# Optimization experiments

Measured on AMD Instinct MI355X. Metric: run time of the kernel, lower is better.

The kernel has to match this reference:

```python
import jax, jax.numpy as jnp
import numpy as np
from jax import lax

CR = 16        # opt.cr (temporal dim)
HEADS = 4      # num_heads
DIM = 64       # dim == channel count c
B = 2          # true batch; input batch = B*CR
H = W = 128


def setup_inputs() -> dict:
    key = jax.random.key(0)
    k1, k2, k3, k4 = jax.random.split(key, 4)
    return {
        "x": jax.random.normal(k1, (B * CR, DIM, H, W), jnp.float32),
        "ln_weight": jnp.ones((DIM,), jnp.float32),
        "ln_bias": jnp.zeros((DIM,), jnp.float32),
        "qkv_w": jax.random.normal(k2, (3 * CR, CR), jnp.float32) * 0.05,   # 1x1 conv
        "dw_w": jax.random.normal(k3, (3 * CR, 1, 3, 3), jnp.float32) * 0.1,  # depthwise 3x3
        "proj_w": jax.random.normal(k4, (DIM, DIM), jnp.float32) * 0.05,   # 1x1 conv
        "temperature": jnp.ones((HEADS, 1, 1), jnp.float32),
    }


def reference(x, ln_weight, ln_bias, qkv_w, dw_w, proj_w, temperature):
    b, c, h, w = x.shape
    Bt = b // CR
    # WithBias LayerNorm over channel dim (per spatial location), eps=1e-5
    mu = jnp.mean(x, axis=1, keepdims=True)
    var = jnp.mean(jnp.square(x - mu), axis=1, keepdims=True)
    xn = (x - mu) / jnp.sqrt(var + 1e-5)
    xn = xn * ln_weight[None, :, None, None] + ln_bias[None, :, None, None]
    # (B*cr, c, h, w) -> (B, cr, c, h, w) -> (B*c, cr, h, w)
    x_in = xn.reshape(Bt, CR, c, h, w).transpose(0, 2, 1, 3, 4).reshape(Bt * c, CR, h, w)
    # 1x1 qkv conv (no bias)
    qkv = jnp.einsum('oc,bchw->bohw', qkv_w, x_in)
    # depthwise 3x3 conv, padding 1
    qkv = lax.conv_general_dilated(qkv, dw_w, (1, 1), 'SAME',
                                   feature_group_count=3 * CR,
                                   dimension_numbers=('NCHW', 'OIHW', 'NCHW'))
    q, k, v = jnp.split(qkv, 3, axis=1)
    ch = CR // HEADS  # per-head channel dim

    def heads(t):
        return t.reshape(Bt * c, HEADS, ch, h * w)

    def l2n(t):
        n = jnp.sqrt(jnp.sum(jnp.square(t), axis=-1, keepdims=True))
        return t / jnp.maximum(n, 1e-12)

    q, k, v = heads(q), heads(k), heads(v)
    q, k = l2n(q), l2n(k)
    # transposed (channel) attention: small ch x ch scores
    attn = jnp.einsum('bhcn,bhdn->bhcd', q, k) * temperature[None]
    attn = jax.nn.softmax(attn, axis=-1)
    out = jnp.einsum('bhcd,bhdn->bhcn', attn, v)  # (B*c, heads, ch, hw)
    # (B*c, cr, h, w) -> (B, c, cr, h, w) -> (B*cr, c, h, w)
    out = out.reshape(Bt * c, CR, h, w).reshape(Bt, c, CR, h, w)
    out = out.transpose(0, 2, 1, 3, 4).reshape(b, c, h, w)
    # 1x1 project_out
    return jnp.einsum('oc,bchw->bohw', proj_w, out)
```

## Files before the change

### kernel.cpp

```cpp
#include <hip/hip_runtime.h>
#include <hip/hip_fp16.h>

__device__ __forceinline__ float2 h2f2(unsigned int u) {
  return __half22float2(__builtin_bit_cast(__half2, u));
}
__device__ __forceinline__ unsigned int f2h2(float a, float b) {
  return __builtin_bit_cast(unsigned int, __floats2half2_rn(a, b));
}

#if __has_builtin(__builtin_amdgcn_fdot2)
typedef _Float16 h2v __attribute__((ext_vector_type(2)));
__device__ __forceinline__ float fdot2(unsigned int a, unsigned int b, float c) {
  return __builtin_amdgcn_fdot2(__builtin_bit_cast(h2v, a),
                                __builtin_bit_cast(h2v, b), c, false);
}
#else
__device__ __forceinline__ float fdot2(unsigned int a, unsigned int b, float c) {
  float2 fa = h2f2(a), fb = h2f2(b);
  return fmaf(fa.y, fb.y, fmaf(fa.x, fb.x, c));
}
#endif

__global__ __launch_bounds__(256) void k_stats(const float2* __restrict__ x2,
                                               float4* __restrict__ stats4) {
  int id = blockIdx.x * 256 + threadIdx.x;
  int bb = id >> 13;
  int jp = id & 8191;
  const float2* xp = x2 + ((size_t)bb << 19) + jp;
  float s0 = 0.f, q0 = 0.f, s1 = 0.f, q1 = 0.f;
#pragma unroll
  for (int ci = 0; ci < 64; ++ci) {
    float2 v = xp[(size_t)ci << 13];
    s0 += v.x; q0 = fmaf(v.x, v.x, q0);
    s1 += v.y; q1 = fmaf(v.y, v.y, q1);
  }
  float mu0 = s0 * (1.f / 64.f), mu1 = s1 * (1.f / 64.f);
  float4 r;
  r.x = mu0; r.y = rsqrtf(fmaf(-mu0, mu0, q0 * (1.f / 64.f)) + 1e-5f);
  r.z = mu1; r.w = rsqrtf(fmaf(-mu1, mu1, q1 * (1.f / 64.f)) + 1e-5f);
  stats4[id] = r;
}

__global__ __launch_bounds__(256) void k_wpack(
    const float* __restrict__ qkvw, const float* __restrict__ dww,
    const float* __restrict__ projw, unsigned int* __restrict__ qkvpk,
    unsigned int* __restrict__ dwpk, unsigned int* __restrict__ projpk) {
  int t = blockIdx.x * 256 + threadIdx.x;
  if (t < 2048) {
    int o = t >> 5, c2 = t & 31;
    projpk[t] = f2h2(projw[(o << 6) + 2 * c2], projw[(o << 6) + 2 * c2 + 1]);
  } else if (t < 2432) {
    int i = t - 2048;
    int ch = i >> 3, tp = i & 7;
    qkvpk[i] = f2h2(qkvw[(ch << 4) + 2 * tp], qkvw[(ch << 4) + 2 * tp + 1]);
  } else if (t < 2648) {
    int i = t - 2432;
    int pl = i / 9, k = i - pl * 9;
    dwpk[i] = f2h2(dww[18 * pl + k], dww[18 * pl + 9 + k]);
  }
}

__global__ __launch_bounds__(256, 6) void k_fused(
    const float* __restrict__ x, const float2* __restrict__ stats2,
    const float* __restrict__ lnw, const float* __restrict__ lnb,
    const unsigned int* __restrict__ qkvpk, const unsigned int* __restrict__ dwpk,
    unsigned int* __restrict__ vbuf, float* __restrict__ Sacc,
    float* __restrict__ Nacc) {
  __shared__ unsigned int pre[4896];
  int tid = threadIdx.x;
  int bc = blockIdx.y, bt = bc >> 6, ci = bc & 63;
  int tx0 = (blockIdx.x & 3) << 5, ty0 = (blockIdx.x >> 2) << 4;
  float lw = lnw[ci], lb = lnb[ci];

  unsigned int wc[3][8];
  int waddr[3];
  {
    size_t xci = ((size_t)(bt * 1024 + ci)) << 14;
    int sbase = bt << 18;
#pragma unroll
    for (int it = 0; it < 3; ++it) {
      int pos = tid + (it << 8);
      bool act = pos < 612;
      int hy = pos / 34, hx = pos - hy * 34;
      int gy = ty0 + hy - 1, gx = tx0 + hx - 1;
      bool ok = act && ((unsigned)gy < 128u) && ((unsigned)gx < 128u);
      waddr[it] = act ? (hy * 34 + hx) : -1;
      int gp = (gy << 7) + gx;
#pragma unroll
      for (int tp = 0; tp < 8; ++tp) {
        unsigned int w = 0;
        if (ok) {
          float x0 = x[xci + ((size_t)(2 * tp) << 20) + gp];
          float x1 = x[xci + ((size_t)(2 * tp + 1) << 20) + gp];
          float2 s0 = stats2[sbase + (2 * tp) * 16384 + gp];
          float2 s1 = stats2[sbase + (2 * tp + 1) * 16384 + gp];
          w = f2h2(fmaf((x0 - s0.x) * s0.y, lw, lb),
                   fmaf((x1 - s1.x) * s1.y, lw, lb));
        }
        wc[it][tp] = w;
      }
    }
  }

  int iy = tid >> 4, jx = tid & 15;
  int dwbase = iy * 34 + 2 * jx;

  for (int m = 0; m < 2; ++m) {
#pragma unroll
    for (int it = 0; it < 3; ++it) {
      if (waddr[it] >= 0) {
#pragma unroll
        for (int pl = 0; pl < 8; ++pl) {
          int cE = 2 * pl;
          int gchE = (cE < 8) ? (8 * m + cE) : (16 + 8 * m + (cE - 8));
          float sE = 0.f, sO = 0.f;
#pragma unroll
          for (int tp = 0; tp < 8; ++tp) {
            sE = fdot2(wc[it][tp], qkvpk[gchE * 8 + tp], sE);
            sO = fdot2(wc[it][tp], qkvpk[(gchE + 1) * 8 + tp], sO);
          }
          pre[pl * 612 + waddr[it]] = f2h2(sE, sO);
        }
      }
    }
    __syncthreads();
    unsigned int qkw[16];
#pragma unroll
    for (int pl = 0; pl < 8; ++pl) {
      int gpl = (pl < 4) ? (4 * m + pl) : (8 + 4 * m + (pl - 4));
      const unsigned int* wp = dwpk + gpl * 9;
      __half2 a0 = __floats2half2_rn(0.f, 0.f), a1 = a0;
      int base = pl * 612 + dwbase;
#pragma unroll
      for (int dy = 0; dy < 3; ++dy) {
        uint2 A = *reinterpret_cast<const uint2*>(&pre[base + dy * 34]);
        uint2 B = *reinterpret_cast<const uint2*>(&pre[base + dy * 34 + 2]);
        __half2 d0 = __builtin_bit_cast(__half2, A.x);
        __half2 d1 = __builtin_bit_cast(__half2, A.y);
        __half2 d2 = __builtin_bit_cast(__half2, B.x);
        __half2 d3 = __builtin_bit_cast(__half2, B.y);
        __half2 w0 = __builtin_bit_cast(__half2, wp[dy * 3 + 0]);
        __half2 w1 = __builtin_bit_cast(__half2, wp[dy * 3 + 1]);
        __half2 w2 = __builtin_bit_cast(__half2, wp[dy * 3 + 2]);
        a0 = __hfma2(w0, d0, a0); a0 = __hfma2(w1, d1, a0); a0 = __hfma2(w2, d2, a0);
        a1 = __hfma2(w0, d1, a1); a1 = __hfma2(w1, d2, a1); a1 = __hfma2(w2, d3, a1);
      }
      unsigned int u0 = __builtin_bit_cast(unsigned int, a0);
      unsigned int u1 = __builtin_bit_cast(unsigned int, a1);
      qkw[2 * pl]     = (u0 & 0xFFFFu) | (u1 << 16);
      qkw[2 * pl + 1] = (u0 >> 16) | (u1 & 0xFFFF0000u);
    }
    __syncthreads();
#pragma unroll
    for (int r = 0; r < 16; ++r) pre[r * 258 + tid] = qkw[r];
    __syncthreads();
    {
      int combo = tid >> 3, pc = tid & 7;
      int hp = combo >> 4, cd = combo & 15, cc = cd >> 2, dd = cd & 3;
      const unsigned int* qrow = pre + (4 * hp + cc) * 258;
      const unsigned int* krow = pre + (8 + 4 * hp + dd) * 258;
      float s = 0.f;
#pragma unroll
      for (int i = 0; i < 16; ++i) {
        uint2 q2 = *reinterpret_cast<const uint2*>(&qrow[2 * pc + (i << 4)]);
        uint2 k2 = *reinterpret_cast<const uint2*>(&krow[2 * pc + (i << 4)]);
        s = fdot2(q2.x, k2.x, s);
        s = fdot2(q2.y, k2.y, s);
      }
      s += __shfl_xor(s, 1); s += __shfl_xor(s, 2); s += __shfl_xor(s, 4);
      if (pc == 0)
        atomicAdd(&Sacc[((bc << 2) + 2 * m + hp) * 16 + cc * 4 + dd], s);
    }
    {
      int row = tid >> 4, pc = tid & 15;
      const unsigned int* rp = pre + row * 258;
      float n = 0.f;
#pragma unroll
      for (int i = 0; i < 8; ++i) {
        uint2 v2 = *reinterpret_cast<const uint2*>(&rp[2 * pc + (i << 5)]);
        n = fdot2(v2.x, v2.x, n);
        n = fdot2(v2.y, v2.y, n);
      }
      n += __shfl_xor(n, 1); n += __shfl_xor(n, 2);
      n += __shfl_xor(n, 4); n += __shfl_xor(n, 8);
      if (pc == 0) {
        int g = (row < 8) ? (8 * m + row) : (16 + 8 * m + (row - 8));
        atomicAdd(&Nacc[(bc << 5) + g], n);
      }
    }
    __syncthreads();
  }

#pragma unroll
  for (int it = 0; it < 3; ++it) {
    if (waddr[it] >= 0) {
#pragma unroll
      for (int pl = 0; pl < 8; ++pl) {
        int gchE = 32 + 2 * pl;
        float sE = 0.f, sO = 0.f;
#pragma unroll
        for (int tp = 0; tp < 8; ++tp) {
          sE = fdot2(wc[it][tp], qkvpk[gchE * 8 + tp], sE);
          sO = fdot2(wc[it][tp], qkvpk[(gchE + 1) * 8 + tp], sO);
        }
        pre[pl * 612 + waddr[it]] = f2h2(sE, sO);
      }
    }
  }
  __syncthreads();
#pragma unroll
  for (int pl = 0; pl < 8; ++pl) {
    const unsigned int* wp = dwpk + (16 + pl) * 9;
    __half2 a0 = __floats2half2_rn(0.f, 0.f), a1 = a0;
    int base = pl * 612 + dwbase;
#pragma unroll
    for (int dy = 0; dy < 3; ++dy) {
      uint2 A = *reinterpret_cast<const uint2*>(&pre[base + dy * 34]);
      uint2 B = *reinterpret_cast<const uint2*>(&pre[base + dy * 34 + 2]);
      __half2 d0 = __builtin_bit_cast(__half2, A.x);
      __half2 d1 = __builtin_bit_cast(__half2, A.y);
      __half2 d2 = __builtin_bit_cast(__half2, B.x);
      __half2 d3 = __builtin_bit_cast(__half2, B.y);
      __half2 w0 = __builtin_bit_cast(__half2, wp[dy * 3 + 0]);
      __half2 w1 = __builtin_bit_cast(__half2, wp[dy * 3 + 1]);
      __half2 w2 = __builtin_bit_cast(__half2, wp[dy * 3 + 2]);
      a0 = __hfma2(w0, d0, a0); a0 = __hfma2(w1, d1, a0); a0 = __hfma2(w2, d2, a0);
      a1 = __hfma2(w0, d1, a1); a1 = __hfma2(w1, d2, a1); a1 = __hfma2(w2, d3, a1);
    }
    uint2 st2;
    st2.x = __builtin_bit_cast(unsigned int, a0);
    st2.y = __builtin_bit_cast(unsigned int, a1);
    size_t idx = ((size_t)(bc * 8 + pl) << 14) +
                 (size_t)((ty0 + iy) << 7) + tx0 + 2 * jx;
    *reinterpret_cast<uint2*>(vbuf + idx) = st2;
  }
}

__global__ __launch_bounds__(256) void k_softmax(
    const float* __restrict__ Sacc, const float* __restrict__ Nacc,
    const float* __restrict__ temp, unsigned int* __restrict__ attnpk) {
  int idx = blockIdx.x * 256 + threadIdx.x;
  if (idx >= 512) return;
  int b = idx >> 2, hd = idx & 3;
  int bt = b >> 6, ci = b & 63;
  float tp = temp[hd];
  float iq[4], ik[4];
#pragma unroll
  for (int c = 0; c < 4; ++c) {
    iq[c] = 1.f / fmaxf(sqrtf(Nacc[(b << 5) + (hd << 2) + c]), 1e-12f);
    ik[c] = 1.f / fmaxf(sqrtf(Nacc[(b << 5) + 16 + (hd << 2) + c]), 1e-12f);
  }
  const float* Sp = Sacc + ((b << 2) + hd) * 16;
#pragma unroll
  for (int c = 0; c < 4; ++c) {
    float l[4];
#pragma unroll
    for (int d = 0; d < 4; ++d) l[d] = Sp[c * 4 + d] * iq[c] * ik[d] * tp;
    float m = fmaxf(fmaxf(l[0], l[1]), fmaxf(l[2], l[3]));
    float e0 = expf(l[0] - m), e1 = expf(l[1] - m);
    float e2 = expf(l[2] - m), e3 = expf(l[3] - m);
    float inv = 1.f / (e0 + e1 + e2 + e3);
    unsigned int* dst = attnpk + ((((bt * 4 + hd) * 4 + c) << 7) + ci * 2);
    dst[0] = f2h2(e0 * inv, e1 * inv);
    dst[1] = f2h2(e2 * inv, e3 * inv);
  }
}

__global__ __launch_bounds__(256) void k_outproj(
    const unsigned int* __restrict__ vbuf, const unsigned int* __restrict__ attnpk,
    const unsigned int* __restrict__ projpk, float* __restrict__ out) {
  int comb = blockIdx.y;
  int bt = comb >> 4, hd = (comb >> 2) & 3, c = comb & 3;
  int px = ((blockIdx.x << 8) + threadIdx.x) << 1;

  const unsigned int* apk = attnpk + (((bt * 4 + hd) * 4 + c) << 7);
  float accA[64], accB[64];
#pragma unroll
  for (int o = 0; o < 64; ++o) { accA[o] = 0.f; accB[o] = 0.f; }

  size_t vbase = ((((size_t)bt * 512) + hd * 2) << 14) + px;
  for (int ci2 = 0; ci2 < 32; ++ci2) {
    size_t off0 = vbase + (((size_t)(2 * ci2) * 8) << 14);
    size_t off1 = off0 + ((size_t)8 << 14);
    uint2 v0a = *reinterpret_cast<const uint2*>(&vbuf[off0]);
    uint2 v0b = *reinterpret_cast<const uint2*>(&vbuf[off0 + (1 << 14)]);
    uint2 v1a = *reinterpret_cast<const uint2*>(&vbuf[off1]);
    uint2 v1b = *reinterpret_cast<const uint2*>(&vbuf[off1 + (1 << 14)]);
    float y0A = fdot2(v0a.x, apk[4 * ci2 + 0], fdot2(v0b.x, apk[4 * ci2 + 1], 0.f));
    float y0B = fdot2(v0a.y, apk[4 * ci2 + 0], fdot2(v0b.y, apk[4 * ci2 + 1], 0.f));
    float y1A = fdot2(v1a.x, apk[4 * ci2 + 2], fdot2(v1b.x, apk[4 * ci2 + 3], 0.f));
    float y1B = fdot2(v1a.y, apk[4 * ci2 + 2], fdot2(v1b.y, apk[4 * ci2 + 3], 0.f));
    unsigned int y2A = f2h2(y0A, y1A);
    unsigned int y2B = f2h2(y0B, y1B);
#pragma unroll
    for (int o = 0; o < 64; ++o) {
      unsigned int w = projpk[(o << 5) + ci2];
      accA[o] = fdot2(y2A, w, accA[o]);
      accB[o] = fdot2(y2B, w, accB[o]);
    }
  }
  float* op = out + (((size_t)comb << 6) << 14) + px;
#pragma unroll
  for (int o = 0; o < 64; ++o)
    *reinterpret_cast<float2*>(&op[(size_t)o << 14]) = make_float2(accA[o], accB[o]);
}

extern "C" void kernel_launch(void* const* d_in, const int* in_sizes, int n_in,
                              void* d_out, int out_size, void* d_ws, size_t ws_size,
                              hipStream_t stream) {
  const float* x = (const float*)d_in[0];
  const float* lnw = (const float*)d_in[1];
  const float* lnb = (const float*)d_in[2];
  const float* qkvw = (const float*)d_in[3];
  const float* dww = (const float*)d_in[4];
  const float* projw = (const float*)d_in[5];
  const float* temp = (const float*)d_in[6];
  float* out = (float*)d_out;

  unsigned int* vbuf = (unsigned int*)d_ws;
  char* tail = (char*)d_ws + 67108864ull;
  float4* stats4 = (float4*)tail;
  float* Sacc = (float*)(tail + 4194304ull);
  float* Nacc = Sacc + 8192;
  unsigned int* attnpk = (unsigned int*)(Nacc + 4096);
  unsigned int* projpk = attnpk + 4096;
  unsigned int* qkvpk = projpk + 2048;
  unsigned int* dwpk = qkvpk + 384;

  hipMemsetAsync(Sacc, 0, (8192 + 4096) * sizeof(float), stream);
  k_stats<<<dim3(1024), dim3(256), 0, stream>>>((const float2*)x, stats4);
  k_wpack<<<dim3(11), dim3(256), 0, stream>>>(qkvw, dww, projw, qkvpk, dwpk, projpk);
  k_fused<<<dim3(32, 128), dim3(256), 0, stream>>>(
      x, (const float2*)stats4, lnw, lnb, qkvpk, dwpk, vbuf, Sacc, Nacc);
  k_softmax<<<dim3(2), dim3(256), 0, stream>>>(Sacc, Nacc, temp, attnpk);
  k_outproj<<<dim3(32, 32), dim3(256), 0, stream>>>(vbuf, attnpk, projpk, out);
}
```

Measured before the change: 209.2 us.

## Process qkv one head at a time with smaller LDS and interleaved LN stats

The fused kernel now loops over four heads, each handling 4 q and 4 k channels, instead of two passes of 8. The V path is split into two chunks of 4 planes. This halves the pre-conv shared buffer and adds a separate qk buffer, removing the register array and one barrier per pass. The LayerNorm stats are rewritten so each time pair is stored as one interleaved float4 and read with a single load. The launch-bounds occupancy hint is dropped, and the extra loop iterations add more barriers and atomics.

```diff
diff --git a/kernel.cpp b/kernel.cpp
--- a/kernel.cpp
+++ b/kernel.cpp
@@ -22,7 +22,7 @@
 #endif
 
 __global__ __launch_bounds__(256) void k_stats(const float2* __restrict__ x2,
-                                               float4* __restrict__ stats4) {
+                                               float2* __restrict__ statsT) {
   int id = blockIdx.x * 256 + threadIdx.x;
   int bb = id >> 13;
   int jp = id & 8191;
@@ -35,10 +35,12 @@
     s1 += v.y; q1 = fmaf(v.y, v.y, q1);
   }
   float mu0 = s0 * (1.f / 64.f), mu1 = s1 * (1.f / 64.f);
-  float4 r;
-  r.x = mu0; r.y = rsqrtf(fmaf(-mu0, mu0, q0 * (1.f / 64.f)) + 1e-5f);
-  r.z = mu1; r.w = rsqrtf(fmaf(-mu1, mu1, q1 * (1.f / 64.f)) + 1e-5f);
-  stats4[id] = r;
+  float r0 = rsqrtf(fmaf(-mu0, mu0, q0 * (1.f / 64.f)) + 1e-5f);
+  float r1 = rsqrtf(fmaf(-mu1, mu1, q1 * (1.f / 64.f)) + 1e-5f);
+  int bt = bb >> 4, t = bb & 15, tp = t >> 1, half = t & 1;
+  size_t base = ((size_t)(bt * 8 + tp) << 14);
+  statsT[((base + 2 * jp) << 1) + half] = make_float2(mu0, r0);
+  statsT[((base + 2 * jp + 1) << 1) + half] = make_float2(mu1, r1);
 }
 
 __global__ __launch_bounds__(256) void k_wpack(
@@ -60,13 +62,14 @@
   }
 }
 
-__global__ __launch_bounds__(256, 6) void k_fused(
-    const float* __restrict__ x, const float2* __restrict__ stats2,
+__global__ __launch_bounds__(256) void k_fused(
+    const float* __restrict__ x, const float4* __restrict__ statsT,
     const float* __restrict__ lnw, const float* __restrict__ lnb,
     const unsigned int* __restrict__ qkvpk, const unsigned int* __restrict__ dwpk,
     unsigned int* __restrict__ vbuf, float* __restrict__ Sacc,
     float* __restrict__ Nacc) {
-  __shared__ unsigned int pre[4896];
+  __shared__ unsigned int pre[2448];
+  __shared__ unsigned int qk[2064];
   int tid = threadIdx.x;
   int bc = blockIdx.y, bt = bc >> 6, ci = bc & 63;
   int tx0 = (blockIdx.x & 3) << 5, ty0 = (blockIdx.x >> 2) << 4;
@@ -76,7 +79,7 @@
   int waddr[3];
   {
     size_t xci = ((size_t)(bt * 1024 + ci)) << 14;
-    int sbase = bt << 18;
+    const float4* stb = statsT + ((size_t)(bt * 8) << 14);
 #pragma unroll
     for (int it = 0; it < 3; ++it) {
       int pos = tid + (it << 8);
@@ -90,12 +93,11 @@
       for (int tp = 0; tp < 8; ++tp) {
         unsigned int w = 0;
         if (ok) {
+          float4 s = stb[((size_t)tp << 14) + gp];
           float x0 = x[xci + ((size_t)(2 * tp) << 20) + gp];
           float x1 = x[xci + ((size_t)(2 * tp + 1) << 20) + gp];
-          float2 s0 = stats2[sbase + (2 * tp) * 16384 + gp];
-          float2 s1 = stats2[sbase + (2 * tp + 1) * 16384 + gp];
-          w = f2h2(fmaf((x0 - s0.x) * s0.y, lw, lb),
-                   fmaf((x1 - s1.x) * s1.y, lw, lb));
+          w = f2h2(fmaf((x0 - s.x) * s.y, lw, lb),
+                   fmaf((x1 - s.z) * s.w, lw, lb));
         }
         wc[it][tp] = w;
       }
@@ -105,14 +107,13 @@
   int iy = tid >> 4, jx = tid & 15;
   int dwbase = iy * 34 + 2 * jx;
 
-  for (int m = 0; m < 2; ++m) {
+  for (int h = 0; h < 4; ++h) {
 #pragma unroll
     for (int it = 0; it < 3; ++it) {
       if (waddr[it] >= 0) {
 #pragma unroll
-        for (int pl = 0; pl < 8; ++pl) {
-          int cE = 2 * pl;
-          int gchE = (cE < 8) ? (8 * m + cE) : (16 + 8 * m + (cE - 8));
+        for (int pl = 0; pl < 4; ++pl) {
+          int gchE = (pl < 2) ? (4 * h + 2 * pl) : (16 + 4 * h + 2 * (pl - 2));
           float sE = 0.f, sO = 0.f;
 #pragma unroll
           for (int tp = 0; tp < 8; ++tp) {
@@ -124,10 +125,9 @@
       }
     }
     __syncthreads();
-    unsigned int qkw[16];
-#pragma unroll
-    for (int pl = 0; pl < 8; ++pl) {
-      int gpl = (pl < 4) ? (4 * m + pl) : (8 + 4 * m + (pl - 4));
+#pragma unroll
+    for (int pl = 0; pl < 4; ++pl) {
+      int gpl = (pl < 2) ? (2 * h + pl) : (8 + 2 * h + (pl - 2));
       const unsigned int* wp = dwpk + gpl * 9;
       __half2 a0 = __floats2half2_rn(0.f, 0.f), a1 = a0;
       int base = pl * 612 + dwbase;
@@ -147,92 +147,92 @@
       }
       unsigned int u0 = __builtin_bit_cast(unsigned int, a0);
       unsigned int u1 = __builtin_bit_cast(unsigned int, a1);
-      qkw[2 * pl]     = (u0 & 0xFFFFu) | (u1 << 16);
-      qkw[2 * pl + 1] = (u0 >> 16) | (u1 & 0xFFFF0000u);
-    }
-    __syncthreads();
-#pragma unroll
-    for (int r = 0; r < 16; ++r) pre[r * 258 + tid] = qkw[r];
+      qk[(2 * pl) * 258 + tid]     = (u0 & 0xFFFFu) | (u1 << 16);
+      qk[(2 * pl + 1) * 258 + tid] = (u0 >> 16) | (u1 & 0xFFFF0000u);
+    }
     __syncthreads();
     {
-      int combo = tid >> 3, pc = tid & 7;
-      int hp = combo >> 4, cd = combo & 15, cc = cd >> 2, dd = cd & 3;
-      const unsigned int* qrow = pre + (4 * hp + cc) * 258;
-      const unsigned int* krow = pre + (8 + 4 * hp + dd) * 258;
+      int combo = tid >> 4, pc = tid & 15;
+      int cc = combo >> 2, dd = combo & 3;
+      const unsigned int* qrow = qk + cc * 258;
+      const unsigned int* krow = qk + (4 + dd) * 258;
       float s = 0.f;
 #pragma unroll
-      for (int i = 0; i < 16; ++i) {
-        uint2 q2 = *reinterpret_cast<const uint2*>(&qrow[2 * pc + (i << 4)]);
-        uint2 k2 = *reinterpret_cast<const uint2*>(&krow[2 * pc + (i << 4)]);
+      for (int i = 0; i < 8; ++i) {
+        uint2 q2 = *reinterpret_cast<const uint2*>(&qrow[2 * pc + (i << 5)]);
+        uint2 k2 = *reinterpret_cast<const uint2*>(&krow[2 * pc + (i << 5)]);
         s = fdot2(q2.x, k2.x, s);
         s = fdot2(q2.y, k2.y, s);
       }
-      s += __shfl_xor(s, 1); s += __shfl_xor(s, 2); s += __shfl_xor(s, 4);
+      s += __shfl_xor(s, 1); s += __shfl_xor(s, 2);
+      s += __shfl_xor(s, 4); s += __shfl_xor(s, 8);
       if (pc == 0)
-        atomicAdd(&Sacc[((bc << 2) + 2 * m + hp) * 16 + cc * 4 + dd], s);
+        atomicAdd(&Sacc[((bc << 2) + h) * 16 + cc * 4 + dd], s);
     }
     {
-      int row = tid >> 4, pc = tid & 15;
-      const unsigned int* rp = pre + row * 258;
+      int row = tid >> 5, pc = tid & 31;
+      const unsigned int* rp = qk + row * 258;
       float n = 0.f;
 #pragma unroll
-      for (int i = 0; i < 8; ++i) {
-        uint2 v2 = *reinterpret_cast<const uint2*>(&rp[2 * pc + (i << 5)]);
+      for (int i = 0; i < 4; ++i) {
+        uint2 v2 = *reinterpret_cast<const uint2*>(&rp[2 * pc + (i << 6)]);
         n = fdot2(v2.x, v2.x, n);
         n = fdot2(v2.y, v2.y, n);
       }
-      n += __shfl_xor(n, 1); n += __shfl_xor(n, 2);
-      n += __shfl_xor(n, 4); n += __shfl_xor(n, 8);
+      n += __shfl_xor(n, 1); n += __shfl_xor(n, 2); n += __shfl_xor(n, 4);
+      n += __shfl_xor(n, 8); n += __shfl_xor(n, 16);
       if (pc == 0) {
-        int g = (row < 8) ? (8 * m + row) : (16 + 8 * m + (row - 8));
+        int g = (row < 4) ? (4 * h + row) : (16 + 4 * h + (row - 4));
         atomicAdd(&Nacc[(bc << 5) + g], n);
       }
     }
+  }
+
+  for (int vc = 0; vc < 2; ++vc) {
+#pragma unroll
+    for (int it = 0; it < 3; ++it) {
+      if (waddr[it] >= 0) {
+#pragma unroll
+        for (int pl = 0; pl < 4; ++pl) {
+          int gchE = 32 + 8 * vc + 2 * pl;
+          float sE = 0.f, sO = 0.f;
+#pragma unroll
+          for (int tp = 0; tp < 8; ++tp) {
+            sE = fdot2(wc[it][tp], qkvpk[gchE * 8 + tp], sE);
+            sO = fdot2(wc[it][tp], qkvpk[(gchE + 1) * 8 + tp], sO);
+          }
+          pre[pl * 612 + waddr[it]] = f2h2(sE, sO);
+        }
+      }
+    }
     __syncthreads();
-  }
-
-#pragma unroll
-  for (int it = 0; it < 3; ++it) {
-    if (waddr[it] >= 0) {
-#pragma unroll
-      for (int pl = 0; pl < 8; ++pl) {
-        int gchE = 32 + 2 * pl;
-        float sE = 0.f, sO = 0.f;
-#pragma unroll
-        for (int tp = 0; tp < 8; ++tp) {
-          sE = fdot2(wc[it][tp], qkvpk[gchE * 8 + tp], sE);
-          sO = fdot2(wc[it][tp], qkvpk[(gchE + 1) * 8 + tp], sO);
-        }
-        pre[pl * 612 + waddr[it]] = f2h2(sE, sO);
-      }
-    }
-  }
-  __syncthreads();
-#pragma unroll
-  for (int pl = 0; pl < 8; ++pl) {
-    const unsigned int* wp = dwpk + (16 + pl) * 9;
-    __half2 a0 = __floats2half2_rn(0.f, 0.f), a1 = a0;
-    int base = pl * 612 + dwbase;
-#pragma unroll
-    for (int dy = 0; dy < 3; ++dy) {
-      uint2 A = *reinterpret_cast<const uint2*>(&pre[base + dy * 34]);
-      uint2 B = *reinterpret_cast<const uint2*>(&pre[base + dy * 34 + 2]);
-      __half2 d0 = __builtin_bit_cast(__half2, A.x);
-      __half2 d1 = __builtin_bit_cast(__half2, A.y);
-      __half2 d2 = __builtin_bit_cast(__half2, B.x);
-      __half2 d3 = __builtin_bit_cast(__half2, B.y);
-      __half2 w0 = __builtin_bit_cast(__half2, wp[dy * 3 + 0]);
-      __half2 w1 = __builtin_bit_cast(__half2, wp[dy * 3 + 1]);
-      __half2 w2 = __builtin_bit_cast(__half2, wp[dy * 3 + 2]);
-      a0 = __hfma2(w0, d0, a0); a0 = __hfma2(w1, d1, a0); a0 = __hfma2(w2, d2, a0);
-      a1 = __hfma2(w0, d1, a1); a1 = __hfma2(w1, d2, a1); a1 = __hfma2(w2, d3, a1);
-    }
-    uint2 st2;
-    st2.x = __builtin_bit_cast(unsigned int, a0);
-    st2.y = __builtin_bit_cast(unsigned int, a1);
-    size_t idx = ((size_t)(bc * 8 + pl) << 14) +
-                 (size_t)((ty0 + iy) << 7) + tx0 + 2 * jx;
-    *reinterpret_cast<uint2*>(vbuf + idx) = st2;
+#pragma unroll
+    for (int pl = 0; pl < 4; ++pl) {
+      const unsigned int* wp = dwpk + (16 + 4 * vc + pl) * 9;
+      __half2 a0 = __floats2half2_rn(0.f, 0.f), a1 = a0;
+      int base = pl * 612 + dwbase;
+#pragma unroll
+      for (int dy = 0; dy < 3; ++dy) {
+        uint2 A = *reinterpret_cast<const uint2*>(&pre[base + dy * 34]);
+        uint2 B = *reinterpret_cast<const uint2*>(&pre[base + dy * 34 + 2]);
+        __half2 d0 = __builtin_bit_cast(__half2, A.x);
+        __half2 d1 = __builtin_bit_cast(__half2, A.y);
+        __half2 d2 = __builtin_bit_cast(__half2, B.x);
+        __half2 d3 = __builtin_bit_cast(__half2, B.y);
+        __half2 w0 = __builtin_bit_cast(__half2, wp[dy * 3 + 0]);
+        __half2 w1 = __builtin_bit_cast(__half2, wp[dy * 3 + 1]);
+        __half2 w2 = __builtin_bit_cast(__half2, wp[dy * 3 + 2]);
+        a0 = __hfma2(w0, d0, a0); a0 = __hfma2(w1, d1, a0); a0 = __hfma2(w2, d2, a0);
+        a1 = __hfma2(w0, d1, a1); a1 = __hfma2(w1, d2, a1); a1 = __hfma2(w2, d3, a1);
+      }
+      uint2 st2;
+      st2.x = __builtin_bit_cast(unsigned int, a0);
+      st2.y = __builtin_bit_cast(unsigned int, a1);
+      size_t idx = ((size_t)(bc * 8 + 4 * vc + pl) << 14) +
+                   (size_t)((ty0 + iy) << 7) + tx0 + 2 * jx;
+      *reinterpret_cast<uint2*>(vbuf + idx) = st2;
+    }
+    if (vc == 0) __syncthreads();
   }
 }
 
@@ -319,7 +319,7 @@
 
   unsigned int* vbuf = (unsigned int*)d_ws;
   char* tail = (char*)d_ws + 67108864ull;
-  float4* stats4 = (float4*)tail;
+  float4* statsT = (float4*)tail;
   float* Sacc = (float*)(tail + 4194304ull);
   float* Nacc = Sacc + 8192;
   unsigned int* attnpk = (unsigned int*)(Nacc + 4096);
@@ -328,10 +328,10 @@
   unsigned int* dwpk = qkvpk + 384;
 
   hipMemsetAsync(Sacc, 0, (8192 + 4096) * sizeof(float), stream);
-  k_stats<<<dim3(1024), dim3(256), 0, stream>>>((const float2*)x, stats4);
+  k_stats<<<dim3(1024), dim3(256), 0, stream>>>((const float2*)x, (float2*)statsT);
   k_wpack<<<dim3(11), dim3(256), 0, stream>>>(qkvw, dww, projw, qkvpk, dwpk, projpk);
   k_fused<<<dim3(32, 128), dim3(256), 0, stream>>>(
-      x, (const float2*)stats4, lnw, lnb, qkvpk, dwpk, vbuf, Sacc, Nacc);
+      x, statsT, lnw, lnb, qkvpk, dwpk, vbuf, Sacc, Nacc);
   k_softmax<<<dim3(2), dim3(256), 0, stream>>>(Sacc, Nacc, temp, attnpk);
   k_outproj<<<dim3(32, 32), dim3(256), 0, stream>>>(vbuf, attnpk, projpk, out);
 }
```

After: 216.6 us. +3.5%, slower.

## Split LayerNorm into packed fp16 pass and use MFMA for qkv conv

Applied to the files above, without the earlier changes.

A new kernel normalizes x and writes it as packed fp16, interleaved so that each pixel's 16 temporal values sit together in a workspace buffer. The fused kernel then reads these packed vectors and computes the 1x1 qkv projection with 16x16x32 f16 MFMA instructions instead of scalar fdot2 loops. The q/k/v loop is merged into three iterations, and the score/norm reductions for the previous stage are overlapped with the next stage through a separate shared buffer. The cost is an extra 64MB intermediate write and read plus one more launch. The MFMA also wastes half its K dimension on zero padding.

```diff
diff --git a/kernel.cpp b/kernel.cpp
--- a/kernel.cpp
+++ b/kernel.cpp
@@ -1,5 +1,8 @@
 #include <hip/hip_runtime.h>
 #include <hip/hip_fp16.h>
+
+typedef _Float16 half8_t __attribute__((ext_vector_type(8)));
+typedef float float4_t __attribute__((ext_vector_type(4)));
 
 __device__ __forceinline__ float2 h2f2(unsigned int u) {
   return __half22float2(__builtin_bit_cast(__half2, u));
@@ -60,74 +63,117 @@
   }
 }
 
-__global__ __launch_bounds__(256, 6) void k_fused(
-    const float* __restrict__ x, const float2* __restrict__ stats2,
+__global__ __launch_bounds__(256) void k_xn(
+    const float2* __restrict__ x2, const float4* __restrict__ stats4,
     const float* __restrict__ lnw, const float* __restrict__ lnb,
-    const unsigned int* __restrict__ qkvpk, const unsigned int* __restrict__ dwpk,
-    unsigned int* __restrict__ vbuf, float* __restrict__ Sacc,
-    float* __restrict__ Nacc) {
-  __shared__ unsigned int pre[4896];
+    unsigned int* __restrict__ xnw) {
+  int bc = blockIdx.y, bt = bc >> 6, ci = bc & 63;
+  int jp = blockIdx.x * 256 + threadIdx.x;
+  float lw = lnw[ci], lb = lnb[ci];
+  unsigned int w0[8], w1[8];
+#pragma unroll
+  for (int tp = 0; tp < 8; ++tp) {
+    int bb0 = (bt << 4) + 2 * tp;
+    float2 xa = x2[(((size_t)((bb0 << 6) + ci)) << 13) + jp];
+    float2 xb = x2[(((size_t)(((bb0 + 1) << 6) + ci)) << 13) + jp];
+    float4 sa = stats4[((size_t)bb0 << 13) + jp];
+    float4 sb = stats4[((size_t)(bb0 + 1) << 13) + jp];
+    w0[tp] = f2h2(fmaf((xa.x - sa.x) * sa.y, lw, lb),
+                  fmaf((xb.x - sb.x) * sb.y, lw, lb));
+    w1[tp] = f2h2(fmaf((xa.y - sa.z) * sa.w, lw, lb),
+                  fmaf((xb.y - sb.z) * sb.w, lw, lb));
+  }
+  size_t base = (((size_t)bc << 14) + 2 * (size_t)jp) * 8;
+  *reinterpret_cast<uint4*>(&xnw[base + 0]) = make_uint4(w0[0], w0[1], w0[2], w0[3]);
+  *reinterpret_cast<uint4*>(&xnw[base + 4]) = make_uint4(w0[4], w0[5], w0[6], w0[7]);
+  *reinterpret_cast<uint4*>(&xnw[base + 8]) = make_uint4(w1[0], w1[1], w1[2], w1[3]);
+  *reinterpret_cast<uint4*>(&xnw[base + 12]) = make_uint4(w1[4], w1[5], w1[6], w1[7]);
+}
+
+__global__ __launch_bounds__(256) void k_fused(
+    const unsigned int* __restrict__ xnw, const unsigned int* __restrict__ qkvpk,
+    const unsigned int* __restrict__ dwpk, unsigned int* __restrict__ vbuf,
+    float* __restrict__ Sacc, float* __restrict__ Nacc) {
+  __shared__ unsigned int pre[8 * 612];
+  __shared__ unsigned int qk[16 * 258];
   int tid = threadIdx.x;
-  int bc = blockIdx.y, bt = bc >> 6, ci = bc & 63;
+  int bc = blockIdx.y;
   int tx0 = (blockIdx.x & 3) << 5, ty0 = (blockIdx.x >> 2) << 4;
-  float lw = lnw[ci], lb = lnb[ci];
-
-  unsigned int wc[3][8];
-  int waddr[3];
-  {
-    size_t xci = ((size_t)(bt * 1024 + ci)) << 14;
-    int sbase = bt << 18;
-#pragma unroll
-    for (int it = 0; it < 3; ++it) {
-      int pos = tid + (it << 8);
-      bool act = pos < 612;
-      int hy = pos / 34, hx = pos - hy * 34;
-      int gy = ty0 + hy - 1, gx = tx0 + hx - 1;
-      bool ok = act && ((unsigned)gy < 128u) && ((unsigned)gx < 128u);
-      waddr[it] = act ? (hy * 34 + hx) : -1;
-      int gp = (gy << 7) + gx;
-#pragma unroll
-      for (int tp = 0; tp < 8; ++tp) {
-        unsigned int w = 0;
-        if (ok) {
-          float x0 = x[xci + ((size_t)(2 * tp) << 20) + gp];
-          float x1 = x[xci + ((size_t)(2 * tp + 1) << 20) + gp];
-          float2 s0 = stats2[sbase + (2 * tp) * 16384 + gp];
-          float2 s1 = stats2[sbase + (2 * tp + 1) * 16384 + gp];
-          w = f2h2(fmaf((x0 - s0.x) * s0.y, lw, lb),
-                   fmaf((x1 - s1.x) * s1.y, lw, lb));
-        }
-        wc[it][tp] = w;
-      }
-    }
-  }
-
+  int lane15 = tid & 15;
+  int kg = (tid >> 4) & 3;
+  int wv = tid >> 6;
   int iy = tid >> 4, jx = tid & 15;
   int dwbase = iy * 34 + 2 * jx;
-
-  for (int m = 0; m < 2; ++m) {
-#pragma unroll
-    for (int it = 0; it < 3; ++it) {
-      if (waddr[it] >= 0) {
-#pragma unroll
-        for (int pl = 0; pl < 8; ++pl) {
-          int cE = 2 * pl;
-          int gchE = (cE < 8) ? (8 * m + cE) : (16 + 8 * m + (cE - 8));
-          float sE = 0.f, sO = 0.f;
-#pragma unroll
-          for (int tp = 0; tp < 8; ++tp) {
-            sE = fdot2(wc[it][tp], qkvpk[gchE * 8 + tp], sE);
-            sO = fdot2(wc[it][tp], qkvpk[(gchE + 1) * 8 + tp], sO);
-          }
-          pre[pl * 612 + waddr[it]] = f2h2(sE, sO);
+  size_t xnbase = (size_t)bc << 17;
+
+  for (int m = 0; m < 3; ++m) {
+    if (m > 0) {
+      int pm = m - 1;
+      {
+        int combo = tid >> 3, pc = tid & 7;
+        int hp_ = combo >> 4, cd = combo & 15, cc = cd >> 2, dd = cd & 3;
+        const unsigned int* qrow = qk + (4 * hp_ + cc) * 258;
+        const unsigned int* krow = qk + (8 + 4 * hp_ + dd) * 258;
+        float s = 0.f;
+#pragma unroll
+        for (int i = 0; i < 16; ++i) {
+          uint2 q2 = *reinterpret_cast<const uint2*>(&qrow[2 * pc + (i << 4)]);
+          uint2 k2 = *reinterpret_cast<const uint2*>(&krow[2 * pc + (i << 4)]);
+          s = fdot2(q2.x, k2.x, s);
+          s = fdot2(q2.y, k2.y, s);
+        }
+        s += __shfl_xor(s, 1); s += __shfl_xor(s, 2); s += __shfl_xor(s, 4);
+        if (pc == 0)
+          atomicAdd(&Sacc[((bc << 2) + 2 * pm + hp_) * 16 + cc * 4 + dd], s);
+      }
+      {
+        int row = tid >> 4, pc = tid & 15;
+        const unsigned int* rp = qk + row * 258;
+        float n = 0.f;
+#pragma unroll
+        for (int i = 0; i < 8; ++i) {
+          uint2 v2 = *reinterpret_cast<const uint2*>(&rp[2 * pc + (i << 5)]);
+          n = fdot2(v2.x, v2.x, n);
+          n = fdot2(v2.y, v2.y, n);
+        }
+        n += __shfl_xor(n, 1); n += __shfl_xor(n, 2);
+        n += __shfl_xor(n, 4); n += __shfl_xor(n, 8);
+        if (pc == 0) {
+          int gidx = (row < 8) ? (8 * pm + row) : (16 + 8 * pm + (row - 8));
+          atomicAdd(&Nacc[(bc << 5) + gidx], n);
+        }
+      }
+    }
+    {
+      int gch = (m < 2)
+                    ? ((lane15 < 8) ? (8 * m + lane15) : (16 + 8 * m + (lane15 - 8)))
+                    : (32 + lane15);
+      uint4 aw = make_uint4(0, 0, 0, 0);
+      if (kg < 2) aw = *reinterpret_cast<const uint4*>(&qkvpk[gch * 8 + 4 * kg]);
+      half8_t af = __builtin_bit_cast(half8_t, aw);
+      float4_t zz = {0.f, 0.f, 0.f, 0.f};
+      for (int T = wv; T < 39; T += 4) {
+        int hp = T * 16 + lane15;
+        int hy = hp / 34, hx = hp - hy * 34;
+        int gy = ty0 + hy - 1, gx = tx0 + hx - 1;
+        bool inb = (hp < 612) && ((unsigned)gy < 128u) && ((unsigned)gx < 128u);
+        uint4 bw = make_uint4(0, 0, 0, 0);
+        if (inb && kg < 2)
+          bw = *reinterpret_cast<const uint4*>(
+              &xnw[xnbase + (size_t)((gy << 7) + gx) * 8 + 4 * kg]);
+        half8_t bf = __builtin_bit_cast(half8_t, bw);
+        float4_t d = __builtin_amdgcn_mfma_f32_16x16x32_f16(af, bf, zz, 0, 0, 0);
+        if (hp < 612) {
+          pre[(2 * kg) * 612 + hp] = f2h2(d[0], d[1]);
+          pre[(2 * kg + 1) * 612 + hp] = f2h2(d[2], d[3]);
         }
       }
     }
     __syncthreads();
-    unsigned int qkw[16];
 #pragma unroll
     for (int pl = 0; pl < 8; ++pl) {
-      int gpl = (pl < 4) ? (4 * m + pl) : (8 + 4 * m + (pl - 4));
+      int gpl = (m < 2) ? ((pl < 4) ? (4 * m + pl) : (8 + 4 * m + (pl - 4)))
+                        : (16 + pl);
       const unsigned int* wp = dwpk + gpl * 9;
       __half2 a0 = __floats2half2_rn(0.f, 0.f), a1 = a0;
       int base = pl * 612 + dwbase;
@@ -147,92 +193,19 @@
       }
       unsigned int u0 = __builtin_bit_cast(unsigned int, a0);
       unsigned int u1 = __builtin_bit_cast(unsigned int, a1);
-      qkw[2 * pl]     = (u0 & 0xFFFFu) | (u1 << 16);
-      qkw[2 * pl + 1] = (u0 >> 16) | (u1 & 0xFFFF0000u);
+      if (m < 2) {
+        qk[(2 * pl) * 258 + tid]     = (u0 & 0xFFFFu) | (u1 << 16);
+        qk[(2 * pl + 1) * 258 + tid] = (u0 >> 16) | (u1 & 0xFFFF0000u);
+      } else {
+        uint2 st2;
+        st2.x = u0;
+        st2.y = u1;
+        size_t idx = ((size_t)(bc * 8 + pl) << 14) +
+                     (size_t)((ty0 + iy) << 7) + tx0 + 2 * jx;
+        *reinterpret_cast<uint2*>(vbuf + idx) = st2;
+      }
     }
-    __syncthreads();
-#pragma unroll
-    for (int r = 0; r < 16; ++r) pre[r * 258 + tid] = qkw[r];
-    __syncthreads();
-    {
-      int combo = tid >> 3, pc = tid & 7;
-      int hp = combo >> 4, cd = combo & 15, cc = cd >> 2, dd = cd & 3;
-      const unsigned int* qrow = pre + (4 * hp + cc) * 258;
-      const unsigned int* krow = pre + (8 + 4 * hp + dd) * 258;
-      float s = 0.f;
-#pragma unroll
-      for (int i = 0; i < 16; ++i) {
-        uint2 q2 = *reinterpret_cast<const uint2*>(&qrow[2 * pc + (i << 4)]);
-        uint2 k2 = *reinterpret_cast<const uint2*>(&krow[2 * pc + (i << 4)]);
-        s = fdot2(q2.x, k2.x, s);
-        s = fdot2(q2.y, k2.y, s);
-      }
-      s += __shfl_xor(s, 1); s += __shfl_xor(s, 2); s += __shfl_xor(s, 4);
-      if (pc == 0)
-        atomicAdd(&Sacc[((bc << 2) + 2 * m + hp) * 16 + cc * 4 + dd], s);
-    }
-    {
-      int row = tid >> 4, pc = tid & 15;
-      const unsigned int* rp = pre + row * 258;
-      float n = 0.f;
-#pragma unroll
-      for (int i = 0; i < 8; ++i) {
-        uint2 v2 = *reinterpret_cast<const uint2*>(&rp[2 * pc + (i << 5)]);
-        n = fdot2(v2.x, v2.x, n);
-        n = fdot2(v2.y, v2.y, n);
-      }
-      n += __shfl_xor(n, 1); n += __shfl_xor(n, 2);
-      n += __shfl_xor(n, 4); n += __shfl_xor(n, 8);
-      if (pc == 0) {
-        int g = (row < 8) ? (8 * m + row) : (16 + 8 * m + (row - 8));
-        atomicAdd(&Nacc[(bc << 5) + g], n);
-      }
-    }
-    __syncthreads();
-  }
-
-#pragma unroll
-  for (int it = 0; it < 3; ++it) {
-    if (waddr[it] >= 0) {
-#pragma unroll
-      for (int pl = 0; pl < 8; ++pl) {
-        int gchE = 32 + 2 * pl;
-        float sE = 0.f, sO = 0.f;
-#pragma unroll
-        for (int tp = 0; tp < 8; ++tp) {
-          sE = fdot2(wc[it][tp], qkvpk[gchE * 8 + tp], sE);
-          sO = fdot2(wc[it][tp], qkvpk[(gchE + 1) * 8 + tp], sO);
-        }
-        pre[pl * 612 + waddr[it]] = f2h2(sE, sO);
-      }
-    }
-  }
-  __syncthreads();
-#pragma unroll
-  for (int pl = 0; pl < 8; ++pl) {
-    const unsigned int* wp = dwpk + (16 + pl) * 9;
-    __half2 a0 = __floats2half2_rn(0.f, 0.f), a1 = a0;
-    int base = pl * 612 + dwbase;
-#pragma unroll
-    for (int dy = 0; dy < 3; ++dy) {
-      uint2 A = *reinterpret_cast<const uint2*>(&pre[base + dy * 34]);
-      uint2 B = *reinterpret_cast<const uint2*>(&pre[base + dy * 34 + 2]);
-      __half2 d0 = __builtin_bit_cast(__half2, A.x);
-      __half2 d1 = __builtin_bit_cast(__half2, A.y);
-      __half2 d2 = __builtin_bit_cast(__half2, B.x);
-      __half2 d3 = __builtin_bit_cast(__half2, B.y);
-      __half2 w0 = __builtin_bit_cast(__half2, wp[dy * 3 + 0]);
-      __half2 w1 = __builtin_bit_cast(__half2, wp[dy * 3 + 1]);
-      __half2 w2 = __builtin_bit_cast(__half2, wp[dy * 3 + 2]);
-      a0 = __hfma2(w0, d0, a0); a0 = __hfma2(w1, d1, a0); a0 = __hfma2(w2, d2, a0);
-      a1 = __hfma2(w0, d1, a1); a1 = __hfma2(w1, d2, a1); a1 = __hfma2(w2, d3, a1);
-    }
-    uint2 st2;
-    st2.x = __builtin_bit_cast(unsigned int, a0);
-    st2.y = __builtin_bit_cast(unsigned int, a1);
-    size_t idx = ((size_t)(bc * 8 + pl) << 14) +
-                 (size_t)((ty0 + iy) << 7) + tx0 + 2 * jx;
-    *reinterpret_cast<uint2*>(vbuf + idx) = st2;
+    if (m < 2) __syncthreads();
   }
 }
 
@@ -317,8 +290,9 @@
   const float* temp = (const float*)d_in[6];
   float* out = (float*)d_out;
 
-  unsigned int* vbuf = (unsigned int*)d_ws;
-  char* tail = (char*)d_ws + 67108864ull;
+  unsigned int* xnw = (unsigned int*)d_ws;
+  unsigned int* vbuf = xnw + (67108864ull / 4);
+  char* tail = (char*)d_ws + 134217728ull;
   float4* stats4 = (float4*)tail;
   float* Sacc = (float*)(tail + 4194304ull);
   float* Nacc = Sacc + 8192;
@@ -330,8 +304,8 @@
   hipMemsetAsync(Sacc, 0, (8192 + 4096) * sizeof(float), stream);
   k_stats<<<dim3(1024), dim3(256), 0, stream>>>((const float2*)x, stats4);
   k_wpack<<<dim3(11), dim3(256), 0, stream>>>(qkvw, dww, projw, qkvpk, dwpk, projpk);
-  k_fused<<<dim3(32, 128), dim3(256), 0, stream>>>(
-      x, (const float2*)stats4, lnw, lnb, qkvpk, dwpk, vbuf, Sacc, Nacc);
+  k_xn<<<dim3(32, 128), dim3(256), 0, stream>>>((const float2*)x, stats4, lnw, lnb, xnw);
+  k_fused<<<dim3(32, 128), dim3(256), 0, stream>>>(xnw, qkvpk, dwpk, vbuf, Sacc, Nacc);
   k_softmax<<<dim3(2), dim3(256), 0, stream>>>(Sacc, Nacc, temp, attnpk);
   k_outproj<<<dim3(32, 32), dim3(256), 0, stream>>>(vbuf, attnpk, projpk, out);
 }
```

New measurement: 234.9 us. +12.3%, slower.
